# Performance work log

Measured on AMD Instinct MI355X. Metric: run time of the kernel, lower is better.

The kernel has to match this reference:

```python
import jax, jax.numpy as jnp
import numpy as np

N_NODES = 100000
N_EDGES = 1600000
D_FEAT = 128
N_CLASSES = 16


def setup_inputs() -> dict:
    key = jax.random.key(0)
    ks = jax.random.split(key, 7)
    return {
        "x": jax.random.normal(ks[0], (N_NODES, D_FEAT), dtype=jnp.float32),
        "edge_row": jax.random.randint(ks[1], (N_EDGES,), 0, N_NODES),
        "edge_col": jax.random.randint(ks[2], (N_EDGES,), 0, N_NODES),
        "edge_val": jax.random.uniform(ks[3], (N_EDGES,), dtype=jnp.float32),
        "w1": jax.random.normal(ks[4], (D_FEAT, D_FEAT), dtype=jnp.float32) * 0.05,
        "w2": jax.random.normal(ks[5], (D_FEAT, D_FEAT), dtype=jnp.float32) * 0.05,
        "classifier": jax.random.normal(ks[6], (D_FEAT, N_CLASSES), dtype=jnp.float32) * 0.05,
    }


def reference(x, edge_row, edge_col, edge_val, w1, w2, classifier):
    n = x.shape[0]

    def spmm(h):
        # Adj.dot(h): gather source node features, scale by edge weight, scatter-add to rows
        msgs = edge_val[:, None] * h[edge_col]          # [E, D]
        return jax.ops.segment_sum(msgs, edge_row, num_segments=n)  # [N, D]

    h = x
    for w in (w1, w2):
        h = jax.nn.relu(spmm(h) @ w)
    logits = h @ classifier                              # [N, C]
    # x[x>0]=1; x[x<=0]=0  -> hard binary threshold
    return jnp.where(logits > 0, jnp.float32(1.0), jnp.float32(0.0))
```

## Files before the change

kernel.cpp:

```cpp
#include <hip/hip_runtime.h>
#include <climits>

#define D 128

typedef float f32x4 __attribute__((ext_vector_type(4)));
typedef int   i32x2 __attribute__((ext_vector_type(2)));

__global__ __launch_bounds__(256) void hist_rank_kernel(const int* __restrict__ erow,
                                                        int* __restrict__ deg,
                                                        int* __restrict__ rank, int nE) {
    int e = blockIdx.x * 256 + threadIdx.x;
    if (e < nE) rank[e] = atomicAdd(&deg[erow[e]], 1);
}

__global__ __launch_bounds__(256) void scan1_kernel(const int* __restrict__ deg,
                                                    int* __restrict__ rowptr,
                                                    int* __restrict__ blocksums, int n) {
    __shared__ int sd[256];
    const int t = threadIdx.x;
    const int idx = blockIdx.x * 1024 + t * 4;
    int4 v = make_int4(0, 0, 0, 0);
    if (idx + 3 < n) v = *(const int4*)&deg[idx];
    else {
        if (idx + 0 < n) v.x = deg[idx + 0];
        if (idx + 1 < n) v.y = deg[idx + 1];
        if (idx + 2 < n) v.z = deg[idx + 2];
        if (idx + 3 < n) v.w = deg[idx + 3];
    }
    v.x = (v.x + 7) & ~7; v.y = (v.y + 7) & ~7;
    v.z = (v.z + 7) & ~7; v.w = (v.w + 7) & ~7;
    const int s = v.x + v.y + v.z + v.w;
    sd[t] = s;
    __syncthreads();
    for (int off = 1; off < 256; off <<= 1) {
        int tv = (t >= off) ? sd[t - off] : 0;
        __syncthreads();
        sd[t] += tv;
        __syncthreads();
    }
    const int excl = sd[t] - s;
    int a = excl + v.x, b = a + v.y, c = b + v.z, d = c + v.w;
    if (idx + 0 < n) rowptr[idx + 1] = a;
    if (idx + 1 < n) rowptr[idx + 2] = b;
    if (idx + 2 < n) rowptr[idx + 3] = c;
    if (idx + 3 < n) rowptr[idx + 4] = d;
    if (t == 255) blocksums[blockIdx.x] = sd[255];
}

__global__ __launch_bounds__(256) void scan2_kernel(int* __restrict__ blocksums, int nb) {
    __shared__ int sd[256];
    const int t = threadIdx.x;
    const int v = (t < nb) ? blocksums[t] : 0;
    sd[t] = v;
    __syncthreads();
    for (int off = 1; off < 256; off <<= 1) {
        int tv = (t >= off) ? sd[t - off] : 0;
        __syncthreads();
        sd[t] += tv;
        __syncthreads();
    }
    if (t < nb) blocksums[t] = sd[t] - v;
}

__global__ __launch_bounds__(256) void scan3_kernel(int* __restrict__ rowptr,
                                                    const int* __restrict__ blocksums, int n) {
    int i = blockIdx.x * 256 + threadIdx.x;
    if (i < n) rowptr[i + 1] += blocksums[i >> 10];
    if (i == 0) rowptr[0] = 0;
}

__global__ __launch_bounds__(256) void place_kernel(const int* __restrict__ erow,
                                                    const int* __restrict__ rank,
                                                    const int* __restrict__ ecol,
                                                    const float* __restrict__ ev,
                                                    const int* __restrict__ rowptr,
                                                    i32x2* __restrict__ cv, int nE) {
    int e = blockIdx.x * 256 + threadIdx.x;
    if (e >= nE) return;
    int pos = rowptr[erow[e]] + rank[e];
    i32x2 rec;
    rec.x = ecol[e];
    rec.y = __float_as_int(ev[e]);
    cv[pos] = rec;
}

__global__ __launch_bounds__(256) void sortrow_wave_kernel(const int* __restrict__ rowptr,
                                                           const int* __restrict__ deg,
                                                           i32x2* __restrict__ cv, int n) {
    int row = blockIdx.x * 4 + (threadIdx.x >> 6);
    if (row >= n) return;
    const int lane = threadIdx.x & 63;
    const int s = rowptr[row], pe = rowptr[row + 1];
    const int dg = deg[row];
    const int npad = pe - s - dg;
    i32x2 zero; zero.x = 0; zero.y = 0;
    if (dg <= 64) {
        unsigned long long key = ~0ull;
        i32x2 rec = zero;
        if (lane < dg) {
            rec = cv[s + lane];
            key = ((unsigned long long)(unsigned)rec.x << 32) | (unsigned)rec.y;
        }
        int rank = 0;
        for (int i = 0; i < dg; ++i) {
            unsigned long long ki = __shfl(key, i);
            rank += (ki < key || (ki == key && i < lane)) ? 1 : 0;
        }
        if (lane < dg) cv[s + rank] = rec;
        if (lane < npad) cv[s + dg + lane] = zero;
    } else if (lane == 0) {
        for (int i = s + 1; i < s + dg; ++i) {
            i32x2 r_ = cv[i];
            unsigned long long k_ = ((unsigned long long)(unsigned)r_.x << 32) | (unsigned)r_.y;
            int j = i - 1;
            while (j >= s) {
                i32x2 rj = cv[j];
                unsigned long long kj = ((unsigned long long)(unsigned)rj.x << 32) | (unsigned)rj.y;
                if (kj <= k_) break;
                cv[j + 1] = rj;
                --j;
            }
            cv[j + 1] = r_;
        }
        for (int i = s + dg; i < pe; ++i) cv[i] = zero;
    }
}

template <bool CLASSIFY>
__global__ __launch_bounds__(256) void spmm_gemm_kernel(
        const float* __restrict__ h, const int* __restrict__ rowptr,
        const i32x2* __restrict__ cv, const float* __restrict__ W,
        const float* __restrict__ Cls, float* __restrict__ O, int n) {
    const int wid = (blockIdx.x * 256 + threadIdx.x) >> 6;
    const int lane = threadIdx.x & 63;
    const int sw = lane >> 5;
    const int l = lane & 31;
    const int row0 = wid * 8;
    if (row0 >= n) return;
    const int rbase = row0 + sw * 4;

    const f32x4* hl = (const f32x4*)h + l;
    f32x4 rowdata[4];

#pragma unroll
    for (int jp = 0; jp < 2; ++jp) {
        const int rA = rbase + jp * 2;
        const int rB = rA + 1;
        int kA = 0, eA = 0, kB = 0, eB = 0;
        if (rA < n) { kA = rowptr[rA]; eA = rowptr[rA + 1]; }
        if (rB < n) { kB = rowptr[rB]; eB = rowptr[rB + 1]; }
        f32x4 accA = (f32x4)(0.f), accB = (f32x4)(0.f);
        while (kA < eA || kB < eB) {
            i32x2 pA[8], pB[8];
            const bool doA = kA < eA, doB = kB < eB;
            if (doA) {
#pragma unroll
                for (int u = 0; u < 8; ++u) pA[u] = cv[kA + u];
            }
            if (doB) {
#pragma unroll
                for (int u = 0; u < 8; ++u) pB[u] = cv[kB + u];
            }
            if (doA) {
                f32x4 hv[8];
#pragma unroll
                for (int u = 0; u < 8; ++u) hv[u] = hl[(size_t)pA[u].x * 32];
#pragma unroll
                for (int u = 0; u < 8; ++u) accA += __int_as_float(pA[u].y) * hv[u];
                kA += 8;
            }
            if (doB) {
                f32x4 hv[8];
#pragma unroll
                for (int u = 0; u < 8; ++u) hv[u] = hl[(size_t)pB[u].x * 32];
#pragma unroll
                for (int u = 0; u < 8; ++u) accB += __int_as_float(pB[u].y) * hv[u];
                kB += 8;
            }
        }
        rowdata[jp * 2]     = accA;
        rowdata[jp * 2 + 1] = accB;
    }

    const int c0 = l * 4;
    const int sbase = sw << 5;
    f32x4 oacc[4];
#pragma unroll
    for (int i = 0; i < 4; ++i) oacc[i] = (f32x4)(0.f);

    for (int k4 = 0; k4 < D / 4; ++k4) {
        const int srcl = sbase + k4;
#pragma unroll
        for (int kk = 0; kk < 4; ++kk) {
            const f32x4 w = *(const f32x4*)&W[(k4 * 4 + kk) * D + c0];
#pragma unroll
            for (int i = 0; i < 4; ++i) {
                float hk = __shfl(rowdata[i][kk], srcl);
                oacc[i] += hk * w;
            }
        }
    }

    if (!CLASSIFY) {
#pragma unroll
        for (int i = 0; i < 4; ++i) {
            const int r = rbase + i;
            if (r < n) {
                f32x4 v;
                v.x = fmaxf(oacc[i].x, 0.f); v.y = fmaxf(oacc[i].y, 0.f);
                v.z = fmaxf(oacc[i].z, 0.f); v.w = fmaxf(oacc[i].w, 0.f);
                *(f32x4*)&O[(size_t)r * D + c0] = v;
            }
        }
    } else {
#pragma unroll
        for (int i = 0; i < 4; ++i) {
            oacc[i].x = fmaxf(oacc[i].x, 0.f); oacc[i].y = fmaxf(oacc[i].y, 0.f);
            oacc[i].z = fmaxf(oacc[i].z, 0.f); oacc[i].w = fmaxf(oacc[i].w, 0.f);
        }
        const int j = l & 15;
        const int kh = l >> 4;
        float lg[4] = {0.f, 0.f, 0.f, 0.f};
        for (int m4 = 0; m4 < 16; ++m4) {
            const int srcl = sbase + kh * 16 + m4;
#pragma unroll
            for (int kk = 0; kk < 4; ++kk) {
                const int k = kh * 64 + m4 * 4 + kk;
                const float c = Cls[k * 16 + j];
#pragma unroll
                for (int i = 0; i < 4; ++i) {
                    float hk = __shfl(oacc[i][kk], srcl);
                    lg[i] += hk * c;
                }
            }
        }
#pragma unroll
        for (int i = 0; i < 4; ++i) lg[i] += __shfl_xor(lg[i], 16);
        if (kh == 0) {
#pragma unroll
            for (int i = 0; i < 4; ++i) {
                const int r = rbase + i;
                if (r < n) O[(size_t)r * 16 + j] = lg[i] > 0.f ? 1.f : 0.f;
            }
        }
    }
}

extern "C" void kernel_launch(void* const* d_in, const int* in_sizes, int n_in,
                              void* d_out, int out_size, void* d_ws, size_t ws_size,
                              hipStream_t stream) {
    const float* x    = (const float*)d_in[0];
    const int*   erow = (const int*)d_in[1];
    const int*   ecol = (const int*)d_in[2];
    const float* ev   = (const float*)d_in[3];
    const float* w1   = (const float*)d_in[4];
    const float* w2   = (const float*)d_in[5];
    const float* cls  = (const float*)d_in[6];

    const int n  = in_sizes[0] / D;
    const int nE = in_sizes[1];

    char*  ws     = (char*)d_ws;
    float* h      = (float*)ws;                 ws += (size_t)n * D * 4;
    int*   deg    = (int*)ws;                   ws += (size_t)n * 4;
    int*   rowptr = (int*)ws;                   ws += (size_t)(n + 1) * 4;
    int*   rank   = (int*)ws;                   ws += (size_t)nE * 4;
    i32x2* cv     = (i32x2*)ws;                 ws += ((size_t)nE + 8 * (size_t)n) * 8;
    int*   bsums  = (int*)ws;                   ws += 256 * 4;

    const int nb = (n + 1023) / 1024;

    dim3 blk(256);
    dim3 egrid((nE + 255) / 256);
    dim3 ngrid((n + 255) / 256);
    dim3 wgrid((n + 3) / 4);
    dim3 sgrid((n + 31) / 32);

    (void)hipMemsetAsync(deg, 0, (size_t)n * 4, stream);
    hist_rank_kernel<<<egrid, blk, 0, stream>>>(erow, deg, rank, nE);
    scan1_kernel<<<nb, blk, 0, stream>>>(deg, rowptr, bsums, n);
    scan2_kernel<<<1, blk, 0, stream>>>(bsums, nb);
    scan3_kernel<<<ngrid, blk, 0, stream>>>(rowptr, bsums, n);
    place_kernel<<<egrid, blk, 0, stream>>>(erow, rank, ecol, ev, rowptr, cv, nE);
    sortrow_wave_kernel<<<wgrid, blk, 0, stream>>>(rowptr, deg, cv, n);

    spmm_gemm_kernel<false><<<sgrid, blk, 0, stream>>>(x, rowptr, cv, w1, nullptr, h, n);

    spmm_gemm_kernel<true><<<sgrid, blk, 0, stream>>>(h, rowptr, cv, w2, cls,
                                                      (float*)d_out, n);
}
```

Baseline: 438.0 us.

## Replace per-row sort with fixed-point integer accumulation for order-independent SpMM

Drops the per-row sort of the CSR entries that existed only to make the floating-point sum order deterministic. The SpMM now scales edge weights by 2^28 and accumulates truncated 64-bit integer products, which gives an order-independent result. It also merges the two scan-fixup kernels into one and zero-fills the padded CSR buffer with a memset instead of in the sort kernel. In exchange it adds float-to-int64 conversions and 64-bit adds in the inner loop, and quantizes each product to about 2^-28, which could flip outputs near the zero threshold.

```diff
diff --git a/kernel.cpp b/kernel.cpp
--- a/kernel.cpp
+++ b/kernel.cpp
@@ -2,6 +2,8 @@
 #include <climits>
 
 #define D 128
+#define FPSCALE 268435456.0f
+#define FPINV   3.7252902984619141e-09f
 
 typedef float f32x4 __attribute__((ext_vector_type(4)));
 typedef int   i32x2 __attribute__((ext_vector_type(2)));
@@ -47,7 +49,9 @@
     if (t == 255) blocksums[blockIdx.x] = sd[255];
 }
 
-__global__ __launch_bounds__(256) void scan2_kernel(int* __restrict__ blocksums, int nb) {
+__global__ __launch_bounds__(256) void scan3_kernel(int* __restrict__ rowptr,
+                                                    const int* __restrict__ blocksums,
+                                                    int n, int nb) {
     __shared__ int sd[256];
     const int t = threadIdx.x;
     const int v = (t < nb) ? blocksums[t] : 0;
@@ -59,13 +63,12 @@
         sd[t] += tv;
         __syncthreads();
     }
-    if (t < nb) blocksums[t] = sd[t] - v;
-}
-
-__global__ __launch_bounds__(256) void scan3_kernel(int* __restrict__ rowptr,
-                                                    const int* __restrict__ blocksums, int n) {
-    int i = blockIdx.x * 256 + threadIdx.x;
-    if (i < n) rowptr[i + 1] += blocksums[i >> 10];
+    const int excl = sd[t] - v;
+    __syncthreads();
+    sd[t] = excl;
+    __syncthreads();
+    int i = blockIdx.x * 256 + t;
+    if (i < n) rowptr[i + 1] += sd[i >> 10];
     if (i == 0) rowptr[0] = 0;
 }
 
@@ -80,50 +83,8 @@
     int pos = rowptr[erow[e]] + rank[e];
     i32x2 rec;
     rec.x = ecol[e];
-    rec.y = __float_as_int(ev[e]);
+    rec.y = __float_as_int(ev[e] * FPSCALE);
     cv[pos] = rec;
-}
-
-__global__ __launch_bounds__(256) void sortrow_wave_kernel(const int* __restrict__ rowptr,
-                                                           const int* __restrict__ deg,
-                                                           i32x2* __restrict__ cv, int n) {
-    int row = blockIdx.x * 4 + (threadIdx.x >> 6);
-    if (row >= n) return;
-    const int lane = threadIdx.x & 63;
-    const int s = rowptr[row], pe = rowptr[row + 1];
-    const int dg = deg[row];
-    const int npad = pe - s - dg;
-    i32x2 zero; zero.x = 0; zero.y = 0;
-    if (dg <= 64) {
-        unsigned long long key = ~0ull;
-        i32x2 rec = zero;
-        if (lane < dg) {
-            rec = cv[s + lane];
-            key = ((unsigned long long)(unsigned)rec.x << 32) | (unsigned)rec.y;
-        }
-        int rank = 0;
-        for (int i = 0; i < dg; ++i) {
-            unsigned long long ki = __shfl(key, i);
-            rank += (ki < key || (ki == key && i < lane)) ? 1 : 0;
-        }
-        if (lane < dg) cv[s + rank] = rec;
-        if (lane < npad) cv[s + dg + lane] = zero;
-    } else if (lane == 0) {
-        for (int i = s + 1; i < s + dg; ++i) {
-            i32x2 r_ = cv[i];
-            unsigned long long k_ = ((unsigned long long)(unsigned)r_.x << 32) | (unsigned)r_.y;
-            int j = i - 1;
-            while (j >= s) {
-                i32x2 rj = cv[j];
-                unsigned long long kj = ((unsigned long long)(unsigned)rj.x << 32) | (unsigned)rj.y;
-                if (kj <= k_) break;
-                cv[j + 1] = rj;
-                --j;
-            }
-            cv[j + 1] = r_;
-        }
-        for (int i = s + dg; i < pe; ++i) cv[i] = zero;
-    }
 }
 
 template <bool CLASSIFY>
@@ -149,7 +110,8 @@
         int kA = 0, eA = 0, kB = 0, eB = 0;
         if (rA < n) { kA = rowptr[rA]; eA = rowptr[rA + 1]; }
         if (rB < n) { kB = rowptr[rB]; eB = rowptr[rB + 1]; }
-        f32x4 accA = (f32x4)(0.f), accB = (f32x4)(0.f);
+        long long aA0 = 0, aA1 = 0, aA2 = 0, aA3 = 0;
+        long long aB0 = 0, aB1 = 0, aB2 = 0, aB3 = 0;
         while (kA < eA || kB < eB) {
             i32x2 pA[8], pB[8];
             const bool doA = kA < eA, doB = kB < eB;
@@ -166,7 +128,13 @@
 #pragma unroll
                 for (int u = 0; u < 8; ++u) hv[u] = hl[(size_t)pA[u].x * 32];
 #pragma unroll
-                for (int u = 0; u < 8; ++u) accA += __int_as_float(pA[u].y) * hv[u];
+                for (int u = 0; u < 8; ++u) {
+                    const float vs = __int_as_float(pA[u].y);
+                    aA0 += (long long)(vs * hv[u].x);
+                    aA1 += (long long)(vs * hv[u].y);
+                    aA2 += (long long)(vs * hv[u].z);
+                    aA3 += (long long)(vs * hv[u].w);
+                }
                 kA += 8;
             }
             if (doB) {
@@ -174,12 +142,23 @@
 #pragma unroll
                 for (int u = 0; u < 8; ++u) hv[u] = hl[(size_t)pB[u].x * 32];
 #pragma unroll
-                for (int u = 0; u < 8; ++u) accB += __int_as_float(pB[u].y) * hv[u];
+                for (int u = 0; u < 8; ++u) {
+                    const float vs = __int_as_float(pB[u].y);
+                    aB0 += (long long)(vs * hv[u].x);
+                    aB1 += (long long)(vs * hv[u].y);
+                    aB2 += (long long)(vs * hv[u].z);
+                    aB3 += (long long)(vs * hv[u].w);
+                }
                 kB += 8;
             }
         }
-        rowdata[jp * 2]     = accA;
-        rowdata[jp * 2 + 1] = accB;
+        f32x4 fA, fB;
+        fA.x = (float)aA0 * FPINV; fA.y = (float)aA1 * FPINV;
+        fA.z = (float)aA2 * FPINV; fA.w = (float)aA3 * FPINV;
+        fB.x = (float)aB0 * FPINV; fB.y = (float)aB1 * FPINV;
+        fB.z = (float)aB2 * FPINV; fB.w = (float)aB3 * FPINV;
+        rowdata[jp * 2]     = fA;
+        rowdata[jp * 2 + 1] = fB;
     }
 
     const int c0 = l * 4;
@@ -269,20 +248,19 @@
     int*   bsums  = (int*)ws;                   ws += 256 * 4;
 
     const int nb = (n + 1023) / 1024;
+    const size_t cv_bytes = ((size_t)nE + 8 * (size_t)n) * 8;
 
     dim3 blk(256);
     dim3 egrid((nE + 255) / 256);
     dim3 ngrid((n + 255) / 256);
-    dim3 wgrid((n + 3) / 4);
     dim3 sgrid((n + 31) / 32);
 
     (void)hipMemsetAsync(deg, 0, (size_t)n * 4, stream);
+    (void)hipMemsetAsync(cv, 0, cv_bytes, stream);
     hist_rank_kernel<<<egrid, blk, 0, stream>>>(erow, deg, rank, nE);
     scan1_kernel<<<nb, blk, 0, stream>>>(deg, rowptr, bsums, n);
-    scan2_kernel<<<1, blk, 0, stream>>>(bsums, nb);
-    scan3_kernel<<<ngrid, blk, 0, stream>>>(rowptr, bsums, n);
+    scan3_kernel<<<ngrid, blk, 0, stream>>>(rowptr, bsums, n, nb);
     place_kernel<<<egrid, blk, 0, stream>>>(erow, rank, ecol, ev, rowptr, cv, nE);
-    sortrow_wave_kernel<<<wgrid, blk, 0, stream>>>(rowptr, deg, cv, n);
 
     spmm_gemm_kernel<false><<<sgrid, blk, 0, stream>>>(x, rowptr, cv, w1, nullptr, h, n);
 
```

New measurement: 455.8 us. 1.04x slower.
